# Kernel optimization log

Hardware: AMD Instinct MI355X
Metric: run time of the kernel (lower is better)

Reference implementation:

```python
import jax, jax.numpy as jnp
import numpy as np

B, L, D, K = 16, 2048, 768, 32
NEG = jnp.float32(-1e30)

def setup_inputs() -> dict:
    key = jax.random.key(0)
    k1, k2, k3, k4 = jax.random.split(key, 4)
    token_hidden = jax.random.normal(k1, (B, L, D), dtype=jnp.float32)
    attention_mask = jnp.ones((B, L), dtype=jnp.float32)
    # ragged spans: sorted boundaries -> contiguous, possibly-empty spans
    bounds = jnp.sort(jax.random.randint(k2, (B, K + 1), 0, L), axis=-1)
    span_starts = bounds[:, :-1].astype(jnp.int32)   # [B, K]
    span_ends = bounds[:, 1:].astype(jnp.int32)      # [B, K]
    w_pool = jax.random.normal(k3, (D,), dtype=jnp.float32) * 0.02
    b_pool = jax.random.normal(k4, (1,), dtype=jnp.float32) * 0.02
    return {"token_hidden": token_hidden, "attention_mask": attention_mask,
            "span_starts": span_starts, "span_ends": span_ends,
            "w_pool": w_pool, "b_pool": b_pool}

def reference(token_hidden, attention_mask, span_starts, span_ends, w_pool, b_pool):
    # sent_pool(vecs): scores per token, shared across spans  -> [B, L]
    scores = jnp.einsum('bld,d->bl', token_hidden, w_pool) + b_pool[0]
    pos = jnp.arange(token_hidden.shape[1], dtype=jnp.int32)  # [L]
    # span membership mask [B, K, L]; empty / out-of-range spans -> all False
    span_mask = ((pos[None, None, :] >= span_starts[:, :, None]) &
                 (pos[None, None, :] < span_ends[:, :, None]) &
                 (attention_mask[:, None, :] >= 0.5))
    logits = jnp.where(span_mask, scores[:, None, :], NEG)  # [B, K, L]
    m = jnp.max(logits, axis=-1, keepdims=True)
    e = jnp.exp(logits - m) * span_mask                      # stable masked softmax
    s = jnp.sum(e, axis=-1, keepdims=True)
    w = e / jnp.maximum(s, jnp.float32(1e-30))               # zero rows for empty spans
    H = jnp.einsum('bkl,bld->bkd', w, token_hidden)          # [B, K, D]
    sent_mask = jnp.any(span_mask, axis=-1).astype(jnp.float32)  # [B, K]
    return H, sent_mask
```

## Files before the change

kernel.cpp:

```cpp
#include <hip/hip_runtime.h>

#define BB 16
#define LL 2048
#define DD 768
#define KK 32
#define NEGI -1e30f
#define JJ 4
#define AW 4
#define SLOTS (JJ * AW)

__global__ __launch_bounds__(256) void span_pool_a(
    const float* __restrict__ th,
    const float* __restrict__ attn,
    const int* __restrict__ sps,
    const int* __restrict__ spe,
    const float* __restrict__ wp,
    float* __restrict__ pacc,
    float* __restrict__ pm,
    float* __restrict__ ps) {
  const int bk = blockIdx.x;
  const int j  = blockIdx.y;
  const int b  = bk >> 5;
  const int lane = threadIdx.x & 63;
  const int wave = threadIdx.x >> 6;
  const int slot = j * AW + wave;

  __shared__ float sacc[AW][DD];
  __shared__ float sm[AW], ss[AW];

  int s0 = min(max(sps[bk], 0), LL);
  int e0 = min(max(spe[bk], 0), LL);

  const float4* wr = (const float4*)wp;
  const float4 w0 = wr[lane], w1 = wr[lane + 64], w2 = wr[lane + 128];

  const float* arow = attn + (size_t)b * LL;
  const float4* tb = (const float4*)(th + (size_t)b * LL * DD);

  float m = NEGI, s = 0.f;
  float4 a0 = make_float4(0.f, 0.f, 0.f, 0.f), a1 = a0, a2 = a0;

  #pragma unroll 2
  for (int l = s0 + slot; l < e0; l += SLOTS) {
    const float4* row = tb + (size_t)l * (DD / 4);
    float4 r0 = row[lane], r1 = row[lane + 64], r2 = row[lane + 128];
    float am = arow[l];

    float d = 0.f;
    d = fmaf(r0.x, w0.x, d); d = fmaf(r0.y, w0.y, d);
    d = fmaf(r0.z, w0.z, d); d = fmaf(r0.w, w0.w, d);
    d = fmaf(r1.x, w1.x, d); d = fmaf(r1.y, w1.y, d);
    d = fmaf(r1.z, w1.z, d); d = fmaf(r1.w, w1.w, d);
    d = fmaf(r2.x, w2.x, d); d = fmaf(r2.y, w2.y, d);
    d = fmaf(r2.z, w2.z, d); d = fmaf(r2.w, w2.w, d);
    #pragma unroll
    for (int o = 32; o > 0; o >>= 1) d += __shfl_xor(d, o, 64);

    if (am >= 0.5f) {
      if (d <= m) {
        const float e = __expf(d - m);
        s += e;
        a0.x = fmaf(e, r0.x, a0.x); a0.y = fmaf(e, r0.y, a0.y);
        a0.z = fmaf(e, r0.z, a0.z); a0.w = fmaf(e, r0.w, a0.w);
        a1.x = fmaf(e, r1.x, a1.x); a1.y = fmaf(e, r1.y, a1.y);
        a1.z = fmaf(e, r1.z, a1.z); a1.w = fmaf(e, r1.w, a1.w);
        a2.x = fmaf(e, r2.x, a2.x); a2.y = fmaf(e, r2.y, a2.y);
        a2.z = fmaf(e, r2.z, a2.z); a2.w = fmaf(e, r2.w, a2.w);
      } else {
        const float sc = __expf(m - d);
        s = fmaf(s, sc, 1.0f);
        a0.x = fmaf(a0.x, sc, r0.x); a0.y = fmaf(a0.y, sc, r0.y);
        a0.z = fmaf(a0.z, sc, r0.z); a0.w = fmaf(a0.w, sc, r0.w);
        a1.x = fmaf(a1.x, sc, r1.x); a1.y = fmaf(a1.y, sc, r1.y);
        a1.z = fmaf(a1.z, sc, r1.z); a1.w = fmaf(a1.w, sc, r1.w);
        a2.x = fmaf(a2.x, sc, r2.x); a2.y = fmaf(a2.y, sc, r2.y);
        a2.z = fmaf(a2.z, sc, r2.z); a2.w = fmaf(a2.w, sc, r2.w);
        m = d;
      }
    }
  }

  float4* sa = (float4*)sacc[wave];
  sa[lane] = a0; sa[lane + 64] = a1; sa[lane + 128] = a2;
  if (lane == 0) { sm[wave] = m; ss[wave] = s; }
  __syncthreads();

  const int t = threadIdx.x;
  if (t < DD / 4) {
    float M = NEGI;
    #pragma unroll
    for (int w = 0; w < AW; ++w) M = fmaxf(M, sm[w]);
    float S = 0.f;
    float4 o = make_float4(0.f, 0.f, 0.f, 0.f);
    #pragma unroll
    for (int w = 0; w < AW; ++w) {
      const float ew = __expf(sm[w] - M);
      S = fmaf(ew, ss[w], S);
      const float4 p = ((const float4*)sacc[w])[t];
      o.x = fmaf(ew, p.x, o.x); o.y = fmaf(ew, p.y, o.y);
      o.z = fmaf(ew, p.z, o.z); o.w = fmaf(ew, p.w, o.w);
    }
    ((float4*)(pacc + (size_t)(bk * JJ + j) * DD))[t] = o;
    if (t == 0) { pm[bk * JJ + j] = M; ps[bk * JJ + j] = S; }
  }
}

__global__ __launch_bounds__(192) void span_pool_b(
    const float* __restrict__ pacc,
    const float* __restrict__ pm,
    const float* __restrict__ ps,
    float* __restrict__ Hout,
    float* __restrict__ sent) {
  const int bk = blockIdx.x;
  const int t = threadIdx.x;

  float mj[JJ], sj[JJ];
  float M = NEGI;
  #pragma unroll
  for (int jv = 0; jv < JJ; ++jv) {
    mj[jv] = pm[bk * JJ + jv];
    sj[jv] = ps[bk * JJ + jv];
    M = fmaxf(M, mj[jv]);
  }
  float S = 0.f;
  #pragma unroll
  for (int jv = 0; jv < JJ; ++jv) S = fmaf(__expf(mj[jv] - M), sj[jv], S);
  const float inv = (S > 0.f) ? (1.0f / S) : 0.f;

  float4 o = make_float4(0.f, 0.f, 0.f, 0.f);
  #pragma unroll
  for (int jv = 0; jv < JJ; ++jv) {
    const float ew = __expf(mj[jv] - M);
    const float4 p = ((const float4*)(pacc + (size_t)(bk * JJ + jv) * DD))[t];
    o.x = fmaf(ew, p.x, o.x); o.y = fmaf(ew, p.y, o.y);
    o.z = fmaf(ew, p.z, o.z); o.w = fmaf(ew, p.w, o.w);
  }
  o.x *= inv; o.y *= inv; o.z *= inv; o.w *= inv;
  ((float4*)(Hout + (size_t)bk * DD))[t] = o;
  if (t == 0) sent[bk] = (S > 0.f) ? 1.0f : 0.0f;
}

extern "C" void kernel_launch(void* const* d_in, const int* in_sizes, int n_in,
                              void* d_out, int out_size, void* d_ws, size_t ws_size,
                              hipStream_t stream) {
  const float* th   = (const float*)d_in[0];
  const float* attn = (const float*)d_in[1];
  const int*   sps  = (const int*)d_in[2];
  const int*   spe  = (const int*)d_in[3];
  const float* wp   = (const float*)d_in[4];

  float* Hout = (float*)d_out;
  float* sent = Hout + (size_t)BB * KK * DD;

  float* pacc = (float*)d_ws;
  float* pm   = pacc + (size_t)BB * KK * JJ * DD;
  float* ps   = pm + (size_t)BB * KK * JJ;

  span_pool_a<<<dim3(BB * KK, JJ), dim3(256), 0, stream>>>(
      th, attn, sps, spe, wp, pacc, pm, ps);
  span_pool_b<<<dim3(BB * KK), dim3(192), 0, stream>>>(
      pacc, pm, ps, Hout, sent);
}
```

Baseline: 175.3 us.

## Precompute token scores in a separate kernel and use two-pass span softmax

Moves the per-token dot product with the pooling weight into its own kernel writing a score buffer, then computes each span's max and sum from those scores before a simple weighted accumulation. This removes the wave-wide shuffle reduction and online-softmax rescaling branches from the main accumulation loop. It also doubles the per-span split factor and unrolls the loop further. The cost is an extra full read of the hidden states and an additional launch.

```diff
diff --git a/kernel.cpp b/kernel.cpp
--- a/kernel.cpp
+++ b/kernel.cpp
@@ -5,135 +5,126 @@
 #define DD 768
 #define KK 32
 #define NEGI -1e30f
-#define JJ 4
+#define JJ 8
 #define AW 4
 #define SLOTS (JJ * AW)
 
-__global__ __launch_bounds__(256) void span_pool_a(
+__global__ __launch_bounds__(256) void span_scores(
     const float* __restrict__ th,
-    const float* __restrict__ attn,
-    const int* __restrict__ sps,
-    const int* __restrict__ spe,
     const float* __restrict__ wp,
-    float* __restrict__ pacc,
-    float* __restrict__ pm,
-    float* __restrict__ ps) {
-  const int bk = blockIdx.x;
-  const int j  = blockIdx.y;
-  const int b  = bk >> 5;
+    float* __restrict__ scores) {
+  const int row  = blockIdx.x * 4 + (threadIdx.x >> 6);
   const int lane = threadIdx.x & 63;
-  const int wave = threadIdx.x >> 6;
-  const int slot = j * AW + wave;
-
-  __shared__ float sacc[AW][DD];
-  __shared__ float sm[AW], ss[AW];
-
-  int s0 = min(max(sps[bk], 0), LL);
-  int e0 = min(max(spe[bk], 0), LL);
 
   const float4* wr = (const float4*)wp;
   const float4 w0 = wr[lane], w1 = wr[lane + 64], w2 = wr[lane + 128];
 
+  const float4* r = (const float4*)(th + (size_t)row * DD);
+  float4 r0 = r[lane], r1 = r[lane + 64], r2 = r[lane + 128];
+
+  float d = 0.f;
+  d = fmaf(r0.x, w0.x, d); d = fmaf(r0.y, w0.y, d);
+  d = fmaf(r0.z, w0.z, d); d = fmaf(r0.w, w0.w, d);
+  d = fmaf(r1.x, w1.x, d); d = fmaf(r1.y, w1.y, d);
+  d = fmaf(r1.z, w1.z, d); d = fmaf(r1.w, w1.w, d);
+  d = fmaf(r2.x, w2.x, d); d = fmaf(r2.y, w2.y, d);
+  d = fmaf(r2.z, w2.z, d); d = fmaf(r2.w, w2.w, d);
+  #pragma unroll
+  for (int o = 32; o > 0; o >>= 1) d += __shfl_xor(d, o, 64);
+
+  if (lane == 0) scores[row] = d;
+}
+
+__global__ __launch_bounds__(256) void span_wsum(
+    const float* __restrict__ th,
+    const float* __restrict__ attn,
+    const float* __restrict__ scores,
+    const int* __restrict__ sps,
+    const int* __restrict__ spe,
+    float* __restrict__ pacc,
+    float* __restrict__ sspan) {
+  const int bk = blockIdx.x;
+  const int j  = blockIdx.y;
+  const int b  = bk >> 5;
+  const int t    = threadIdx.x;
+  const int lane = t & 63;
+  const int wave = t >> 6;
+  const int slot = j * AW + wave;
+
+  __shared__ float sacc[AW][DD];
+  __shared__ float redm[AW], reds[AW];
+
+  const int s0 = min(max(sps[bk], 0), LL);
+  const int e0 = min(max(spe[bk], 0), LL);
+
+  const float* sc   = scores + (size_t)b * LL;
   const float* arow = attn + (size_t)b * LL;
-  const float4* tb = (const float4*)(th + (size_t)b * LL * DD);
+  const float4* tb  = (const float4*)(th + (size_t)b * LL * DD);
 
-  float m = NEGI, s = 0.f;
+  float lm = NEGI;
+  for (int l = s0 + t; l < e0; l += 256)
+    if (arow[l] >= 0.5f) lm = fmaxf(lm, sc[l]);
+  #pragma unroll
+  for (int o = 32; o > 0; o >>= 1) lm = fmaxf(lm, __shfl_xor(lm, o, 64));
+  if (lane == 0) redm[wave] = lm;
+  __syncthreads();
+  const float M = fmaxf(fmaxf(redm[0], redm[1]), fmaxf(redm[2], redm[3]));
+
+  float ls = 0.f;
+  for (int l = s0 + t; l < e0; l += 256)
+    if (arow[l] >= 0.5f) ls += __expf(sc[l] - M);
+  #pragma unroll
+  for (int o = 32; o > 0; o >>= 1) ls += __shfl_xor(ls, o, 64);
+  if (lane == 0) reds[wave] = ls;
+  __syncthreads();
+  const float S = reds[0] + reds[1] + reds[2] + reds[3];
+  if (j == 0 && t == 0) sspan[bk] = S;
+
   float4 a0 = make_float4(0.f, 0.f, 0.f, 0.f), a1 = a0, a2 = a0;
-
-  #pragma unroll 2
+  #pragma unroll 4
   for (int l = s0 + slot; l < e0; l += SLOTS) {
     const float4* row = tb + (size_t)l * (DD / 4);
     float4 r0 = row[lane], r1 = row[lane + 64], r2 = row[lane + 128];
-    float am = arow[l];
-
-    float d = 0.f;
-    d = fmaf(r0.x, w0.x, d); d = fmaf(r0.y, w0.y, d);
-    d = fmaf(r0.z, w0.z, d); d = fmaf(r0.w, w0.w, d);
-    d = fmaf(r1.x, w1.x, d); d = fmaf(r1.y, w1.y, d);
-    d = fmaf(r1.z, w1.z, d); d = fmaf(r1.w, w1.w, d);
-    d = fmaf(r2.x, w2.x, d); d = fmaf(r2.y, w2.y, d);
-    d = fmaf(r2.z, w2.z, d); d = fmaf(r2.w, w2.w, d);
-    #pragma unroll
-    for (int o = 32; o > 0; o >>= 1) d += __shfl_xor(d, o, 64);
-
-    if (am >= 0.5f) {
-      if (d <= m) {
-        const float e = __expf(d - m);
-        s += e;
-        a0.x = fmaf(e, r0.x, a0.x); a0.y = fmaf(e, r0.y, a0.y);
-        a0.z = fmaf(e, r0.z, a0.z); a0.w = fmaf(e, r0.w, a0.w);
-        a1.x = fmaf(e, r1.x, a1.x); a1.y = fmaf(e, r1.y, a1.y);
-        a1.z = fmaf(e, r1.z, a1.z); a1.w = fmaf(e, r1.w, a1.w);
-        a2.x = fmaf(e, r2.x, a2.x); a2.y = fmaf(e, r2.y, a2.y);
-        a2.z = fmaf(e, r2.z, a2.z); a2.w = fmaf(e, r2.w, a2.w);
-      } else {
-        const float sc = __expf(m - d);
-        s = fmaf(s, sc, 1.0f);
-        a0.x = fmaf(a0.x, sc, r0.x); a0.y = fmaf(a0.y, sc, r0.y);
-        a0.z = fmaf(a0.z, sc, r0.z); a0.w = fmaf(a0.w, sc, r0.w);
-        a1.x = fmaf(a1.x, sc, r1.x); a1.y = fmaf(a1.y, sc, r1.y);
-        a1.z = fmaf(a1.z, sc, r1.z); a1.w = fmaf(a1.w, sc, r1.w);
-        a2.x = fmaf(a2.x, sc, r2.x); a2.y = fmaf(a2.y, sc, r2.y);
-        a2.z = fmaf(a2.z, sc, r2.z); a2.w = fmaf(a2.w, sc, r2.w);
-        m = d;
-      }
-    }
+    float e = __expf(sc[l] - M);
+    e = (arow[l] >= 0.5f) ? e : 0.f;
+    a0.x = fmaf(e, r0.x, a0.x); a0.y = fmaf(e, r0.y, a0.y);
+    a0.z = fmaf(e, r0.z, a0.z); a0.w = fmaf(e, r0.w, a0.w);
+    a1.x = fmaf(e, r1.x, a1.x); a1.y = fmaf(e, r1.y, a1.y);
+    a1.z = fmaf(e, r1.z, a1.z); a1.w = fmaf(e, r1.w, a1.w);
+    a2.x = fmaf(e, r2.x, a2.x); a2.y = fmaf(e, r2.y, a2.y);
+    a2.z = fmaf(e, r2.z, a2.z); a2.w = fmaf(e, r2.w, a2.w);
   }
 
   float4* sa = (float4*)sacc[wave];
   sa[lane] = a0; sa[lane + 64] = a1; sa[lane + 128] = a2;
-  if (lane == 0) { sm[wave] = m; ss[wave] = s; }
   __syncthreads();
-
-  const int t = threadIdx.x;
   if (t < DD / 4) {
-    float M = NEGI;
-    #pragma unroll
-    for (int w = 0; w < AW; ++w) M = fmaxf(M, sm[w]);
-    float S = 0.f;
     float4 o = make_float4(0.f, 0.f, 0.f, 0.f);
     #pragma unroll
     for (int w = 0; w < AW; ++w) {
-      const float ew = __expf(sm[w] - M);
-      S = fmaf(ew, ss[w], S);
       const float4 p = ((const float4*)sacc[w])[t];
-      o.x = fmaf(ew, p.x, o.x); o.y = fmaf(ew, p.y, o.y);
-      o.z = fmaf(ew, p.z, o.z); o.w = fmaf(ew, p.w, o.w);
+      o.x += p.x; o.y += p.y; o.z += p.z; o.w += p.w;
     }
     ((float4*)(pacc + (size_t)(bk * JJ + j) * DD))[t] = o;
-    if (t == 0) { pm[bk * JJ + j] = M; ps[bk * JJ + j] = S; }
   }
 }
 
-__global__ __launch_bounds__(192) void span_pool_b(
+__global__ __launch_bounds__(192) void span_merge(
     const float* __restrict__ pacc,
-    const float* __restrict__ pm,
-    const float* __restrict__ ps,
+    const float* __restrict__ sspan,
     float* __restrict__ Hout,
     float* __restrict__ sent) {
   const int bk = blockIdx.x;
   const int t = threadIdx.x;
 
-  float mj[JJ], sj[JJ];
-  float M = NEGI;
-  #pragma unroll
-  for (int jv = 0; jv < JJ; ++jv) {
-    mj[jv] = pm[bk * JJ + jv];
-    sj[jv] = ps[bk * JJ + jv];
-    M = fmaxf(M, mj[jv]);
-  }
-  float S = 0.f;
-  #pragma unroll
-  for (int jv = 0; jv < JJ; ++jv) S = fmaf(__expf(mj[jv] - M), sj[jv], S);
+  const float S = sspan[bk];
   const float inv = (S > 0.f) ? (1.0f / S) : 0.f;
 
   float4 o = make_float4(0.f, 0.f, 0.f, 0.f);
   #pragma unroll
   for (int jv = 0; jv < JJ; ++jv) {
-    const float ew = __expf(mj[jv] - M);
     const float4 p = ((const float4*)(pacc + (size_t)(bk * JJ + jv) * DD))[t];
-    o.x = fmaf(ew, p.x, o.x); o.y = fmaf(ew, p.y, o.y);
-    o.z = fmaf(ew, p.z, o.z); o.w = fmaf(ew, p.w, o.w);
+    o.x += p.x; o.y += p.y; o.z += p.z; o.w += p.w;
   }
   o.x *= inv; o.y *= inv; o.z *= inv; o.w *= inv;
   ((float4*)(Hout + (size_t)bk * DD))[t] = o;
@@ -152,12 +143,13 @@
   float* Hout = (float*)d_out;
   float* sent = Hout + (size_t)BB * KK * DD;
 
-  float* pacc = (float*)d_ws;
-  float* pm   = pacc + (size_t)BB * KK * JJ * DD;
-  float* ps   = pm + (size_t)BB * KK * JJ;
+  float* scores = (float*)d_ws;
+  float* pacc   = scores + (size_t)BB * LL;
+  float* sspan  = pacc + (size_t)BB * KK * JJ * DD;
 
-  span_pool_a<<<dim3(BB * KK, JJ), dim3(256), 0, stream>>>(
-      th, attn, sps, spe, wp, pacc, pm, ps);
-  span_pool_b<<<dim3(BB * KK), dim3(192), 0, stream>>>(
-      pacc, pm, ps, Hout, sent);
+  span_scores<<<dim3(BB * LL / 4), dim3(256), 0, stream>>>(th, wp, scores);
+  span_wsum<<<dim3(BB * KK, JJ), dim3(256), 0, stream>>>(
+      th, attn, scores, sps, spe, pacc, sspan);
+  span_merge<<<dim3(BB * KK), dim3(192), 0, stream>>>(
+      pacc, sspan, Hout, sent);
 }
```

After: 173.1 us. No clear change (-1.3%).
